# Optimization experiments

Hardware: AMD Instinct MI355X
Metric: run time of the kernel (lower is better)

Reference implementation:

```python
import jax, jax.numpy as jnp
import numpy as np

N_NODES = 100000
N_EDGES = 1600000
IN_DIM = 128
OUT_DIM = 32
N_HEADS = 4
NEG_SLOPE = 0.2  # DGL GATConv default LeakyReLU negative slope


def setup_inputs() -> dict:
    key = jax.random.key(0)
    k_h, k_src, k_dst, k_w, k_al, k_ar = jax.random.split(key, 6)
    h = jax.random.normal(k_h, (N_NODES, IN_DIM), dtype=jnp.float32)
    src = jax.random.randint(k_src, (N_EDGES,), 0, N_NODES, dtype=jnp.int32)
    dst = jnp.sort(jax.random.randint(k_dst, (N_EDGES,), 0, N_NODES, dtype=jnp.int32))
    # Xavier-ish init scale
    W = jax.random.normal(k_w, (IN_DIM, N_HEADS * OUT_DIM), dtype=jnp.float32) / np.sqrt(IN_DIM)
    attn_l = jax.random.normal(k_al, (N_HEADS, OUT_DIM), dtype=jnp.float32) / np.sqrt(OUT_DIM)
    attn_r = jax.random.normal(k_ar, (N_HEADS, OUT_DIM), dtype=jnp.float32) / np.sqrt(OUT_DIM)
    bias = jnp.zeros((N_HEADS * OUT_DIM,), dtype=jnp.float32)
    return {"h": h, "src": src, "dst": dst, "W": W, "attn_l": attn_l, "attn_r": attn_r, "bias": bias}


def reference(h, src, dst, W, attn_l, attn_r, bias):
    # Eval-mode GATConv (feat_drop / attn_drop disabled).
    N = h.shape[0]
    # Linear projection -> [N, H, D]
    feat = (h @ W).reshape(N, N_HEADS, OUT_DIM)
    # Per-node attention logits: el/er [N, H]
    el = jnp.einsum('nhd,hd->nh', feat, attn_l)
    er = jnp.einsum('nhd,hd->nh', feat, attn_r)
    # Edge scores: e = LeakyReLU(el[src] + er[dst])  -> [E, H]
    e = el[src] + er[dst]
    e = jnp.where(e > 0, e, NEG_SLOPE * e)
    # Segment softmax over incoming edges of each destination node
    e_max = jax.ops.segment_max(e, dst, num_segments=N, indices_are_sorted=True)
    e_exp = jnp.exp(e - e_max[dst])
    denom = jax.ops.segment_sum(e_exp, dst, num_segments=N, indices_are_sorted=True)
    alpha = e_exp / denom[dst]  # [E, H]
    # Weighted aggregate: sum_e alpha[e] * feat[src[e]] per destination
    msg = feat[src] * alpha[:, :, None]  # [E, H, D]
    rst = jax.ops.segment_sum(msg, dst, num_segments=N, indices_are_sorted=True)  # [N, H, D]
    # Bias + ReLU activation (GATLayer default activation=F.relu)
    rst = rst + bias.reshape(1, N_HEADS, OUT_DIM)
    return jax.nn.relu(rst)
```

## Files before the change

### kernel.cpp

```cpp
#include <hip/hip_runtime.h>
#include <hip/hip_fp16.h>
#include <math.h>

#define NEG_SLOPE 0.2f

typedef _Float16 f16x2 __attribute__((ext_vector_type(2)));
typedef _Float16 f16x8 __attribute__((ext_vector_type(8)));
typedef float f32x4 __attribute__((ext_vector_type(4)));

__device__ __forceinline__ float fdot2f(unsigned int a, unsigned int b, float c) {
#if __has_builtin(__builtin_amdgcn_fdot2)
    return __builtin_amdgcn_fdot2(__builtin_bit_cast(f16x2, a),
                                  __builtin_bit_cast(f16x2, b), c, false);
#else
    __half2 ah = __builtin_bit_cast(__half2, a), bh = __builtin_bit_cast(__half2, b);
    float2 af = __half22float2(ah), bf = __half22float2(bh);
    return c + af.x * bf.x + af.y * bf.y;
#endif
}

__device__ __forceinline__ unsigned int packw(float a, float b) {
#if __has_builtin(__builtin_amdgcn_cvt_pkrtz)
    return __builtin_bit_cast(unsigned int, __builtin_amdgcn_cvt_pkrtz(a, b));
#else
    return __builtin_bit_cast(unsigned int, __floats2half2_rn(a, b));
#endif
}

__global__ __launch_bounds__(256) void prep_seg_kernel(
    const float* __restrict__ W, __half* __restrict__ w16t,
    const int* __restrict__ dst, int* __restrict__ off, int E, int N)
{
    const int b = blockIdx.x;
    if (b < 64) {
        int tid = b * 256 + threadIdx.x;
        int c = tid >> 7, k = tid & 127;
        w16t[c * 128 + k] = __float2half(W[k * 128 + c]);
        return;
    }
    int i = (b - 64) * 256 + threadIdx.x;
    if (i >= E) return;
    int d = dst[i];
    int prev = (i == 0) ? -1 : dst[i - 1];
    for (int n = prev + 1; n <= d; ++n) off[n] = i;
    if (i == E - 1) {
        for (int n = d + 1; n <= N; ++n) off[n] = E;
    }
}

__global__ __launch_bounds__(256) void proj_kernel(
    const float* __restrict__ h, const __half* __restrict__ w16t,
    const float* __restrict__ attn_l, const float* __restrict__ attn_r,
    __half* __restrict__ feat, float* __restrict__ el, float* __restrict__ er,
    int N)
{
    __shared__ __half hl[64 * 128];
    __shared__ __half wl[128 * 128];
    const int t = threadIdx.x;
    const int nodeBase = blockIdx.x * 64;

#pragma unroll
    for (int i = 0; i < 8; ++i) {
        int ch = t + i * 256;
        int col = ch >> 4, k8 = ch & 15;
        uint4 v = *(const uint4*)(w16t + col * 128 + k8 * 8);
        int byte = col * 256 + k8 * 16;
        *(uint4*)((char*)wl + (byte ^ ((col & 7) << 4))) = v;
    }
#pragma unroll
    for (int i = 0; i < 8; ++i) {
        int slot = t + i * 256;
        int row = slot >> 5, c4 = slot & 31;
        int gn = nodeBase + row;
        float4 v = make_float4(0.f, 0.f, 0.f, 0.f);
        if (gn < N) v = *(const float4*)(h + (size_t)gn * 128 + c4 * 4);
        __half2 p0 = __floats2half2_rn(v.x, v.y);
        __half2 p1 = __floats2half2_rn(v.z, v.w);
        uint2 u = make_uint2(__builtin_bit_cast(unsigned int, p0),
                             __builtin_bit_cast(unsigned int, p1));
        int byte = row * 256 + c4 * 8;
        *(uint2*)((char*)hl + (byte ^ ((row & 7) << 4))) = u;
    }
    __syncthreads();

    const int l = t & 63, wave = t >> 6;
    const int arow = wave * 16 + (l & 15);
    const int kg = l >> 4;
    f32x4 acc[8];
#pragma unroll
    for (int i = 0; i < 8; ++i) acc[i] = (f32x4){0.f, 0.f, 0.f, 0.f};

#pragma unroll
    for (int kt = 0; kt < 4; ++kt) {
        const int kb = (kt * 32 + kg * 8) * 2;
        f16x8 a = *(const f16x8*)((const char*)hl +
                    ((arow * 256 + kb) ^ ((arow & 7) << 4)));
#pragma unroll
        for (int ct = 0; ct < 8; ++ct) {
            int bcol = ct * 16 + (l & 15);
            f16x8 b = *(const f16x8*)((const char*)wl +
                        ((bcol * 256 + kb) ^ ((bcol & 7) << 4)));
            acc[ct] = __builtin_amdgcn_mfma_f32_16x16x32_f16(a, b, acc[ct], 0, 0, 0);
        }
    }

    __syncthreads();
    const int colLo = l & 15;
    const int rowHi = wave * 16 + (l >> 4) * 4;
#pragma unroll
    for (int ct = 0; ct < 8; ++ct) {
#pragma unroll
        for (int r = 0; r < 4; ++r) {
            int row = rowHi + r;
            int byte = row * 256 + (ct * 16 + colLo) * 2;
            *(__half*)((char*)hl + (byte ^ ((row & 7) << 4))) = __float2half(acc[ct][r]);
        }
    }

    float pl[4][4], pr[4][4];
#pragma unroll
    for (int hh = 0; hh < 4; ++hh) {
        float al0 = attn_l[hh * 32 + colLo];
        float al1 = attn_l[hh * 32 + 16 + colLo];
        float ar0 = attn_r[hh * 32 + colLo];
        float ar1 = attn_r[hh * 32 + 16 + colLo];
#pragma unroll
        for (int r = 0; r < 4; ++r) {
            pl[hh][r] = acc[2 * hh][r] * al0 + acc[2 * hh + 1][r] * al1;
            pr[hh][r] = acc[2 * hh][r] * ar0 + acc[2 * hh + 1][r] * ar1;
        }
    }
#pragma unroll
    for (int msk = 1; msk <= 8; msk <<= 1) {
#pragma unroll
        for (int hh = 0; hh < 4; ++hh)
#pragma unroll
            for (int r = 0; r < 4; ++r) {
                pl[hh][r] += __shfl_xor(pl[hh][r], msk);
                pr[hh][r] += __shfl_xor(pr[hh][r], msk);
            }
    }
    if (colLo == 0) {
#pragma unroll
        for (int r = 0; r < 4; ++r) {
            int node = nodeBase + rowHi + r;
            if (node < N) {
                *(float4*)(el + (size_t)node * 4) =
                    make_float4(pl[0][r], pl[1][r], pl[2][r], pl[3][r]);
                *(float4*)(er + (size_t)node * 4) =
                    make_float4(pr[0][r], pr[1][r], pr[2][r], pr[3][r]);
            }
        }
    }
    __syncthreads();

    char* featB = (char*)feat + (size_t)nodeBase * 256;
#pragma unroll
    for (int i = 0; i < 4; ++i) {
        int c = t + i * 256;
        int row = c >> 4;
        uint4 v = *(const uint4*)((const char*)hl + ((c * 16) ^ ((row & 7) << 4)));
        if (nodeBase + row < N) *(uint4*)(featB + c * 16) = v;
    }
}

__global__ __launch_bounds__(256) void aggregate_kernel(
    const __half* __restrict__ feat, const float* __restrict__ el,
    const float* __restrict__ er, const int* __restrict__ off,
    const int* __restrict__ src, const float* __restrict__ bias,
    float* __restrict__ out, int N)
{
    const int wid = (int)((blockIdx.x * blockDim.x + threadIdx.x) >> 6);
    const int l = threadIdx.x & 63;
    if (wid >= N) return;
    const int n = __builtin_amdgcn_readfirstlane(wid);
    const int s = off[n];
    const int e = off[n + 1];
    const int f0 = 2 * l;
    const int hm = l >> 4;
    const float b0 = bias[f0], b1 = bias[f0 + 1];
    float* outp = out + (size_t)n * 128;
    if (s >= e) {
        outp[f0] = fmaxf(b0, 0.f);
        outp[f0 + 1] = fmaxf(b1, 0.f);
        return;
    }

    const float er_mine = er[n * 4 + hm];
    float ax = 0.f, ay = 0.f, dn = 0.f;
    const unsigned int one2 = 0x3C003C00u;

    int ei = s;
    for (; ei + 16 <= e; ei += 16) {
        int sv[16];
#pragma unroll
        for (int k = 0; k < 16; ++k) sv[k] = src[ei + k];
        float elv[16];
#pragma unroll
        for (int k = 0; k < 16; ++k) elv[k] = el[(size_t)sv[k] * 4 + hm];
        unsigned int g[16];
#pragma unroll
        for (int k = 0; k < 16; ++k)
            g[k] = *(const unsigned int*)(feat + (size_t)sv[k] * 128 + f0);
        float w[16];
#pragma unroll
        for (int k = 0; k < 16; ++k) {
            float sc = elv[k] + er_mine;
            sc = sc > 0.f ? sc : NEG_SLOPE * sc;
            w[k] = __expf(sc);
        }
#pragma unroll
        for (int k = 0; k < 8; ++k) {
            unsigned int w2 = packw(w[2 * k], w[2 * k + 1]);
            unsigned int lo = __builtin_amdgcn_perm(g[2 * k + 1], g[2 * k], 0x05040100u);
            unsigned int hi = __builtin_amdgcn_perm(g[2 * k + 1], g[2 * k], 0x07060302u);
            ax = fdot2f(w2, lo, ax);
            ay = fdot2f(w2, hi, ay);
            dn = fdot2f(w2, one2, dn);
        }
    }
    if (ei + 8 <= e) {
        int sv[8];
#pragma unroll
        for (int k = 0; k < 8; ++k) sv[k] = src[ei + k];
        float elv[8];
#pragma unroll
        for (int k = 0; k < 8; ++k) elv[k] = el[(size_t)sv[k] * 4 + hm];
        unsigned int g[8];
#pragma unroll
        for (int k = 0; k < 8; ++k)
            g[k] = *(const unsigned int*)(feat + (size_t)sv[k] * 128 + f0);
        float w[8];
#pragma unroll
        for (int k = 0; k < 8; ++k) {
            float sc = elv[k] + er_mine;
            sc = sc > 0.f ? sc : NEG_SLOPE * sc;
            w[k] = __expf(sc);
        }
#pragma unroll
        for (int k = 0; k < 4; ++k) {
            unsigned int w2 = packw(w[2 * k], w[2 * k + 1]);
            unsigned int lo = __builtin_amdgcn_perm(g[2 * k + 1], g[2 * k], 0x05040100u);
            unsigned int hi = __builtin_amdgcn_perm(g[2 * k + 1], g[2 * k], 0x07060302u);
            ax = fdot2f(w2, lo, ax);
            ay = fdot2f(w2, hi, ay);
            dn = fdot2f(w2, one2, dn);
        }
        ei += 8;
    }
    if (ei + 4 <= e) {
        int sv0 = src[ei], sv1 = src[ei + 1], sv2 = src[ei + 2], sv3 = src[ei + 3];
        float e0 = el[(size_t)sv0 * 4 + hm], e1 = el[(size_t)sv1 * 4 + hm];
        float e2 = el[(size_t)sv2 * 4 + hm], e3 = el[(size_t)sv3 * 4 + hm];
        unsigned int g0 = *(const unsigned int*)(feat + (size_t)sv0 * 128 + f0);
        unsigned int g1 = *(const unsigned int*)(feat + (size_t)sv1 * 128 + f0);
        unsigned int g2 = *(const unsigned int*)(feat + (size_t)sv2 * 128 + f0);
        unsigned int g3 = *(const unsigned int*)(feat + (size_t)sv3 * 128 + f0);
        float s0 = e0 + er_mine, s1 = e1 + er_mine, s2 = e2 + er_mine, s3 = e3 + er_mine;
        s0 = s0 > 0.f ? s0 : NEG_SLOPE * s0;
        s1 = s1 > 0.f ? s1 : NEG_SLOPE * s1;
        s2 = s2 > 0.f ? s2 : NEG_SLOPE * s2;
        s3 = s3 > 0.f ? s3 : NEG_SLOPE * s3;
        unsigned int w2a = packw(__expf(s0), __expf(s1));
        unsigned int w2b = packw(__expf(s2), __expf(s3));
        unsigned int lo = __builtin_amdgcn_perm(g1, g0, 0x05040100u);
        unsigned int hi = __builtin_amdgcn_perm(g1, g0, 0x07060302u);
        ax = fdot2f(w2a, lo, ax); ay = fdot2f(w2a, hi, ay); dn = fdot2f(w2a, one2, dn);
        lo = __builtin_amdgcn_perm(g3, g2, 0x05040100u);
        hi = __builtin_amdgcn_perm(g3, g2, 0x07060302u);
        ax = fdot2f(w2b, lo, ax); ay = fdot2f(w2b, hi, ay); dn = fdot2f(w2b, one2, dn);
        ei += 4;
    }
    for (; ei < e; ++ei) {
        int sv = src[ei];
        float sc = el[(size_t)sv * 4 + hm] + er_mine;
        sc = sc > 0.f ? sc : NEG_SLOPE * sc;
        float w = __expf(sc);
        __half2 gh = *(const __half2*)(feat + (size_t)sv * 128 + f0);
        float2 fv = __half22float2(gh);
        ax += w * fv.x; ay += w * fv.y; dn += w;
    }
    const float inv = 1.f / dn;
    *(float2*)(outp + f0) = make_float2(fmaxf(ax * inv + b0, 0.f),
                                        fmaxf(ay * inv + b1, 0.f));
}

extern "C" void kernel_launch(void* const* d_in, const int* in_sizes, int n_in,
                              void* d_out, int out_size, void* d_ws, size_t ws_size,
                              hipStream_t stream)
{
    const float* h      = (const float*)d_in[0];
    const int*   src    = (const int*)d_in[1];
    const int*   dst    = (const int*)d_in[2];
    const float* W      = (const float*)d_in[3];
    const float* attn_l = (const float*)d_in[4];
    const float* attn_r = (const float*)d_in[5];
    const float* bias   = (const float*)d_in[6];
    const int N = in_sizes[0] / 128;
    const int E = in_sizes[1];
    float* out = (float*)d_out;

    char* ws = (char*)d_ws;
    __half* feat = (__half*)ws;            ws += (size_t)N * 128 * sizeof(__half);
    float*  el   = (float*)ws;             ws += (size_t)N * 4 * sizeof(float);
    float*  er   = (float*)ws;             ws += (size_t)N * 4 * sizeof(float);
    __half* w16t = (__half*)ws;            ws += 128 * 128 * sizeof(__half);
    int*    off  = (int*)ws;

    hipLaunchKernelGGL(prep_seg_kernel, dim3(64 + (E + 255) / 256), dim3(256), 0, stream,
                       W, w16t, dst, off, E, N);
    hipLaunchKernelGGL(proj_kernel, dim3((N + 63) / 64), dim3(256), 0, stream,
                       h, w16t, attn_l, attn_r, feat, el, er, N);
    hipLaunchKernelGGL(aggregate_kernel, dim3((N + 3) / 4), dim3(256), 0, stream,
                       feat, el, er, off, src, bias, out, N);
}
```

Measured before the change: 108.9 us.

## Quantize projected features to int8 with per-node scale and cooperative edge weights

The projection kernel now stores features as int8 with one absmax scale per node instead of fp16, halving the bytes gathered per edge in the aggregation. The aggregation kernel also has lanes compute edge weights cooperatively (one el load and exp per lane-edge-head pair), then broadcasts them via shuffles and reduces the denominator with xor shuffles. This replaces the per-lane redundant el gathers and exps. It adds shuffle overhead, an extra scale gather and int8 quantization error in the output.

```diff
diff --git a/kernel.cpp b/kernel.cpp
--- a/kernel.cpp
+++ b/kernel.cpp
@@ -4,28 +4,8 @@
 
 #define NEG_SLOPE 0.2f
 
-typedef _Float16 f16x2 __attribute__((ext_vector_type(2)));
 typedef _Float16 f16x8 __attribute__((ext_vector_type(8)));
 typedef float f32x4 __attribute__((ext_vector_type(4)));
-
-__device__ __forceinline__ float fdot2f(unsigned int a, unsigned int b, float c) {
-#if __has_builtin(__builtin_amdgcn_fdot2)
-    return __builtin_amdgcn_fdot2(__builtin_bit_cast(f16x2, a),
-                                  __builtin_bit_cast(f16x2, b), c, false);
-#else
-    __half2 ah = __builtin_bit_cast(__half2, a), bh = __builtin_bit_cast(__half2, b);
-    float2 af = __half22float2(ah), bf = __half22float2(bh);
-    return c + af.x * bf.x + af.y * bf.y;
-#endif
-}
-
-__device__ __forceinline__ unsigned int packw(float a, float b) {
-#if __has_builtin(__builtin_amdgcn_cvt_pkrtz)
-    return __builtin_bit_cast(unsigned int, __builtin_amdgcn_cvt_pkrtz(a, b));
-#else
-    return __builtin_bit_cast(unsigned int, __floats2half2_rn(a, b));
-#endif
-}
 
 __global__ __launch_bounds__(256) void prep_seg_kernel(
     const float* __restrict__ W, __half* __restrict__ w16t,
@@ -51,8 +31,8 @@
 __global__ __launch_bounds__(256) void proj_kernel(
     const float* __restrict__ h, const __half* __restrict__ w16t,
     const float* __restrict__ attn_l, const float* __restrict__ attn_r,
-    __half* __restrict__ feat, float* __restrict__ el, float* __restrict__ er,
-    int N)
+    signed char* __restrict__ feat8, float* __restrict__ scale,
+    float* __restrict__ el, float* __restrict__ er, int N)
 {
     __shared__ __half hl[64 * 128];
     __shared__ __half wl[128 * 128];
@@ -154,21 +134,58 @@
     }
     __syncthreads();
 
-    char* featB = (char*)feat + (size_t)nodeBase * 256;
-#pragma unroll
-    for (int i = 0; i < 4; ++i) {
-        int c = t + i * 256;
-        int row = c >> 4;
-        uint4 v = *(const uint4*)((const char*)hl + ((c * 16) ^ ((row & 7) << 4)));
-        if (nodeBase + row < N) *(uint4*)(featB + c * 16) = v;
+    {
+        const int r = t >> 2, q = t & 3;
+        uint4 c4[4];
+#pragma unroll
+        for (int j = 0; j < 4; ++j) {
+            int ch = r * 16 + q * 4 + j;
+            c4[j] = *(const uint4*)((const char*)hl + ((ch * 16) ^ ((r & 7) << 4)));
+        }
+        float mx = 1e-20f;
+#pragma unroll
+        for (int j = 0; j < 4; ++j) {
+            const __half2* hp = (const __half2*)&c4[j];
+#pragma unroll
+            for (int u = 0; u < 4; ++u) {
+                float2 f = __half22float2(hp[u]);
+                mx = fmaxf(mx, fmaxf(fabsf(f.x), fabsf(f.y)));
+            }
+        }
+        mx = fmaxf(mx, __shfl_xor(mx, 1));
+        mx = fmaxf(mx, __shfl_xor(mx, 2));
+        const float qinv = 127.f / mx;
+        const int node = nodeBase + r;
+        if (q == 0 && node < N) scale[node] = mx * (1.f / 127.f);
+        unsigned int outw[8];
+#pragma unroll
+        for (int j = 0; j < 4; ++j) {
+            const __half2* hp = (const __half2*)&c4[j];
+#pragma unroll
+            for (int u = 0; u < 2; ++u) {
+                float2 fa = __half22float2(hp[2 * u]);
+                float2 fb = __half22float2(hp[2 * u + 1]);
+                int i0 = __float2int_rn(fa.x * qinv) & 255;
+                int i1 = __float2int_rn(fa.y * qinv) & 255;
+                int i2 = __float2int_rn(fb.x * qinv) & 255;
+                int i3 = __float2int_rn(fb.y * qinv) & 255;
+                outw[j * 2 + u] = (unsigned)i0 | ((unsigned)i1 << 8) |
+                                  ((unsigned)i2 << 16) | ((unsigned)i3 << 24);
+            }
+        }
+        if (node < N) {
+            uint4* d4 = (uint4*)(feat8 + (size_t)node * 128 + q * 32);
+            d4[0] = make_uint4(outw[0], outw[1], outw[2], outw[3]);
+            d4[1] = make_uint4(outw[4], outw[5], outw[6], outw[7]);
+        }
     }
 }
 
 __global__ __launch_bounds__(256) void aggregate_kernel(
-    const __half* __restrict__ feat, const float* __restrict__ el,
-    const float* __restrict__ er, const int* __restrict__ off,
-    const int* __restrict__ src, const float* __restrict__ bias,
-    float* __restrict__ out, int N)
+    const signed char* __restrict__ feat8, const float* __restrict__ scale,
+    const float* __restrict__ el, const float* __restrict__ er,
+    const int* __restrict__ off, const int* __restrict__ src,
+    const float* __restrict__ bias, float* __restrict__ out, int N)
 {
     const int wid = (int)((blockIdx.x * blockDim.x + threadIdx.x) >> 6);
     const int l = threadIdx.x & 63;
@@ -187,98 +204,80 @@
     }
 
     const float er_mine = er[n * 4 + hm];
+    const float er_coop = er[n * 4 + (l & 3)];
     float ax = 0.f, ay = 0.f, dn = 0.f;
-    const unsigned int one2 = 0x3C003C00u;
 
     int ei = s;
     for (; ei + 16 <= e; ei += 16) {
         int sv[16];
 #pragma unroll
         for (int k = 0; k < 16; ++k) sv[k] = src[ei + k];
-        float elv[16];
-#pragma unroll
-        for (int k = 0; k < 16; ++k) elv[k] = el[(size_t)sv[k] * 4 + hm];
-        unsigned int g[16];
+        int svc = src[ei + (l >> 2)];
+        float scl = scale[svc];
+        float sc = el[(size_t)svc * 4 + (l & 3)] + er_coop;
+        sc = sc > 0.f ? sc : NEG_SLOPE * sc;
+        float w = __expf(sc);
+        float ws = w * scl;
+        unsigned short gg[16];
 #pragma unroll
         for (int k = 0; k < 16; ++k)
-            g[k] = *(const unsigned int*)(feat + (size_t)sv[k] * 128 + f0);
-        float w[16];
+            gg[k] = *(const unsigned short*)(feat8 + (size_t)sv[k] * 128 + f0);
+        float dsum = w;
+        dsum += __shfl_xor(dsum, 4);
+        dsum += __shfl_xor(dsum, 8);
+        dsum += __shfl_xor(dsum, 16);
+        dsum += __shfl_xor(dsum, 32);
+        dn += __shfl(dsum, hm);
 #pragma unroll
         for (int k = 0; k < 16; ++k) {
-            float sc = elv[k] + er_mine;
-            sc = sc > 0.f ? sc : NEG_SLOPE * sc;
-            w[k] = __expf(sc);
-        }
-#pragma unroll
-        for (int k = 0; k < 8; ++k) {
-            unsigned int w2 = packw(w[2 * k], w[2 * k + 1]);
-            unsigned int lo = __builtin_amdgcn_perm(g[2 * k + 1], g[2 * k], 0x05040100u);
-            unsigned int hi = __builtin_amdgcn_perm(g[2 * k + 1], g[2 * k], 0x07060302u);
-            ax = fdot2f(w2, lo, ax);
-            ay = fdot2f(w2, hi, ay);
-            dn = fdot2f(w2, one2, dn);
+            float wsk = __shfl(ws, 4 * k + hm);
+            int q0 = (int)(signed char)(gg[k] & 0xff);
+            int q1 = (int)(signed char)(gg[k] >> 8);
+            ax += wsk * (float)q0;
+            ay += wsk * (float)q1;
         }
     }
     if (ei + 8 <= e) {
         int sv[8];
 #pragma unroll
         for (int k = 0; k < 8; ++k) sv[k] = src[ei + k];
-        float elv[8];
-#pragma unroll
-        for (int k = 0; k < 8; ++k) elv[k] = el[(size_t)sv[k] * 4 + hm];
-        unsigned int g[8];
+        int svc = src[ei + ((l >> 2) & 7)];
+        float scl = scale[svc];
+        float sc = el[(size_t)svc * 4 + (l & 3)] + er_coop;
+        sc = sc > 0.f ? sc : NEG_SLOPE * sc;
+        float w = __expf(sc);
+        float ws = w * scl;
+        unsigned short gg[8];
 #pragma unroll
         for (int k = 0; k < 8; ++k)
-            g[k] = *(const unsigned int*)(feat + (size_t)sv[k] * 128 + f0);
-        float w[8];
+            gg[k] = *(const unsigned short*)(feat8 + (size_t)sv[k] * 128 + f0);
+        float dsum = w;
+        dsum += __shfl_xor(dsum, 4);
+        dsum += __shfl_xor(dsum, 8);
+        dsum += __shfl_xor(dsum, 16);
+        dn += __shfl(dsum, hm);
 #pragma unroll
         for (int k = 0; k < 8; ++k) {
-            float sc = elv[k] + er_mine;
-            sc = sc > 0.f ? sc : NEG_SLOPE * sc;
-            w[k] = __expf(sc);
-        }
-#pragma unroll
-        for (int k = 0; k < 4; ++k) {
-            unsigned int w2 = packw(w[2 * k], w[2 * k + 1]);
-            unsigned int lo = __builtin_amdgcn_perm(g[2 * k + 1], g[2 * k], 0x05040100u);
-            unsigned int hi = __builtin_amdgcn_perm(g[2 * k + 1], g[2 * k], 0x07060302u);
-            ax = fdot2f(w2, lo, ax);
-            ay = fdot2f(w2, hi, ay);
-            dn = fdot2f(w2, one2, dn);
+            float wsk = __shfl(ws, 4 * k + hm);
+            int q0 = (int)(signed char)(gg[k] & 0xff);
+            int q1 = (int)(signed char)(gg[k] >> 8);
+            ax += wsk * (float)q0;
+            ay += wsk * (float)q1;
         }
         ei += 8;
-    }
-    if (ei + 4 <= e) {
-        int sv0 = src[ei], sv1 = src[ei + 1], sv2 = src[ei + 2], sv3 = src[ei + 3];
-        float e0 = el[(size_t)sv0 * 4 + hm], e1 = el[(size_t)sv1 * 4 + hm];
-        float e2 = el[(size_t)sv2 * 4 + hm], e3 = el[(size_t)sv3 * 4 + hm];
-        unsigned int g0 = *(const unsigned int*)(feat + (size_t)sv0 * 128 + f0);
-        unsigned int g1 = *(const unsigned int*)(feat + (size_t)sv1 * 128 + f0);
-        unsigned int g2 = *(const unsigned int*)(feat + (size_t)sv2 * 128 + f0);
-        unsigned int g3 = *(const unsigned int*)(feat + (size_t)sv3 * 128 + f0);
-        float s0 = e0 + er_mine, s1 = e1 + er_mine, s2 = e2 + er_mine, s3 = e3 + er_mine;
-        s0 = s0 > 0.f ? s0 : NEG_SLOPE * s0;
-        s1 = s1 > 0.f ? s1 : NEG_SLOPE * s1;
-        s2 = s2 > 0.f ? s2 : NEG_SLOPE * s2;
-        s3 = s3 > 0.f ? s3 : NEG_SLOPE * s3;
-        unsigned int w2a = packw(__expf(s0), __expf(s1));
-        unsigned int w2b = packw(__expf(s2), __expf(s3));
-        unsigned int lo = __builtin_amdgcn_perm(g1, g0, 0x05040100u);
-        unsigned int hi = __builtin_amdgcn_perm(g1, g0, 0x07060302u);
-        ax = fdot2f(w2a, lo, ax); ay = fdot2f(w2a, hi, ay); dn = fdot2f(w2a, one2, dn);
-        lo = __builtin_amdgcn_perm(g3, g2, 0x05040100u);
-        hi = __builtin_amdgcn_perm(g3, g2, 0x07060302u);
-        ax = fdot2f(w2b, lo, ax); ay = fdot2f(w2b, hi, ay); dn = fdot2f(w2b, one2, dn);
-        ei += 4;
     }
     for (; ei < e; ++ei) {
         int sv = src[ei];
         float sc = el[(size_t)sv * 4 + hm] + er_mine;
         sc = sc > 0.f ? sc : NEG_SLOPE * sc;
         float w = __expf(sc);
-        __half2 gh = *(const __half2*)(feat + (size_t)sv * 128 + f0);
-        float2 fv = __half22float2(gh);
-        ax += w * fv.x; ay += w * fv.y; dn += w;
+        float ws = w * scale[sv];
+        unsigned short gg = *(const unsigned short*)(feat8 + (size_t)sv * 128 + f0);
+        int q0 = (int)(signed char)(gg & 0xff);
+        int q1 = (int)(signed char)(gg >> 8);
+        dn += w;
+        ax += ws * (float)q0;
+        ay += ws * (float)q1;
     }
     const float inv = 1.f / dn;
     *(float2*)(outp + f0) = make_float2(fmaxf(ax * inv + b0, 0.f),
@@ -301,16 +300,17 @@
     float* out = (float*)d_out;
 
     char* ws = (char*)d_ws;
-    __half* feat = (__half*)ws;            ws += (size_t)N * 128 * sizeof(__half);
-    float*  el   = (float*)ws;             ws += (size_t)N * 4 * sizeof(float);
-    float*  er   = (float*)ws;             ws += (size_t)N * 4 * sizeof(float);
-    __half* w16t = (__half*)ws;            ws += 128 * 128 * sizeof(__half);
-    int*    off  = (int*)ws;
+    signed char* feat8 = (signed char*)ws;  ws += (size_t)N * 128;
+    float*  scale = (float*)ws;             ws += (size_t)N * sizeof(float);
+    float*  el    = (float*)ws;             ws += (size_t)N * 4 * sizeof(float);
+    float*  er    = (float*)ws;             ws += (size_t)N * 4 * sizeof(float);
+    __half* w16t  = (__half*)ws;            ws += 128 * 128 * sizeof(__half);
+    int*    off   = (int*)ws;
 
     hipLaunchKernelGGL(prep_seg_kernel, dim3(64 + (E + 255) / 256), dim3(256), 0, stream,
                        W, w16t, dst, off, E, N);
     hipLaunchKernelGGL(proj_kernel, dim3((N + 63) / 64), dim3(256), 0, stream,
-                       h, w16t, attn_l, attn_r, feat, el, er, N);
+                       h, w16t, attn_l, attn_r, feat8, scale, el, er, N);
     hipLaunchKernelGGL(aggregate_kernel, dim3((N + 3) / 4), dim3(256), 0, stream,
-                       feat, el, er, off, src, bias, out, N);
+                       feat8, scale, el, er, off, src, bias, out, N);
 }
```

Result: slower. 117.3 us (+7.7%).
